# Kernel optimization log

Hardware: AMD Instinct MI355X
Metric: run time of the kernel (lower is better)

The kernel has to match this reference:

```python
import jax, jax.numpy as jnp
import numpy as np

C, I, O = 32, 1024, 1024
B, T = 64, 512


def setup_inputs() -> dict:
    key = jax.random.key(0)
    kx, kc, kw, kb = jax.random.split(key, 4)
    x = jax.random.normal(kx, (B, T, I), dtype=jnp.float32)
    cat_ids = jax.random.randint(kc, (B,), 0, C)
    W = 0.02 * jax.random.normal(kw, (C, I, O), dtype=jnp.float32)
    b = jnp.zeros((C, O), dtype=jnp.float32)
    return {"x": x, "cat_ids": cat_ids, "W": W, "b": b}


def reference(x, cat_ids, W, b):
    # Per-category affine: y[b] = x[b] @ W[cat_ids[b]] + b[cat_ids[b]]
    selected_W = W[cat_ids]            # [B, I, O] (gathered per batch element)
    selected_b = b[cat_ids]            # [B, O]
    if x.ndim == 2:
        return jnp.einsum('bi,bio->bo', x, selected_W) + selected_b
    return jnp.einsum('bti,bio->bto', x, selected_W) + selected_b[:, None, :]
```

## Files before the change

kernel.cpp:

```cpp
#include <hip/hip_runtime.h>
#include <hip/hip_bf16.h>
#include <stdint.h>

#define CATS  32
#define DI    1024
#define DO    1024
#define NB    64
#define ST    512

typedef float  f32x4  __attribute__((ext_vector_type(4)));
typedef short  bf16x8 __attribute__((ext_vector_type(8)));

__device__ __forceinline__ unsigned short f2bf(float f) {
    union { float f; unsigned int u; } v;
    v.f = f;
    unsigned int r = v.u + 0x7FFFu + ((v.u >> 16) & 1u);
    return (unsigned short)(r >> 16);
}

__global__ __launch_bounds__(256) void wt_transpose_kernel(
        const float* __restrict__ W, unsigned short* __restrict__ Wt) {
    __shared__ float tile[128 * 65];
    const int c  = blockIdx.z;
    const int i0 = blockIdx.y * 128;
    const int o0 = blockIdx.x * 64;
    const float* Wc = W + (size_t)c * DI * DO;
    const int tid = threadIdx.x;

    const int f  = tid & 15;
    const int r0 = tid >> 4;
    #pragma unroll
    for (int rr = 0; rr < 8; ++rr) {
        const int r = r0 + rr * 16;
        const f32x4 v = *(const f32x4*)(Wc + (size_t)(i0 + r) * DO + (o0 + 4 * f));
        #pragma unroll
        for (int j = 0; j < 4; ++j)
            tile[r * 65 + 4 * f + j] = v[j];
    }
    __syncthreads();

    const int g   = tid & 15;
    const int ol0 = tid >> 4;
    unsigned short* WtC = Wt + (size_t)c * DO * DI;
    #pragma unroll
    for (int oo = 0; oo < 4; ++oo) {
        const int ol = ol0 + oo * 16;
        unsigned int w[4];
        #pragma unroll
        for (int j = 0; j < 4; ++j) {
            const unsigned short lo = f2bf(tile[(8 * g + 2 * j + 0) * 65 + ol]);
            const unsigned short hi = f2bf(tile[(8 * g + 2 * j + 1) * 65 + ol]);
            w[j] = (unsigned int)lo | ((unsigned int)hi << 16);
        }
        uint4 pk; pk.x = w[0]; pk.y = w[1]; pk.z = w[2]; pk.w = w[3];
        *(uint4*)(WtC + (size_t)(o0 + ol) * DI + (i0 + 8 * g)) = pk;
    }
}

__global__ __launch_bounds__(256) void x_convert_kernel(
        const float* __restrict__ x, unsigned short* __restrict__ xb) {
    const size_t i = ((size_t)blockIdx.x * 256 + threadIdx.x) * 8;
    const f32x4 v0 = *(const f32x4*)(x + i);
    const f32x4 v1 = *(const f32x4*)(x + i + 4);
    uint4 pk;
    pk.x = (unsigned int)f2bf(v0[0]) | ((unsigned int)f2bf(v0[1]) << 16);
    pk.y = (unsigned int)f2bf(v0[2]) | ((unsigned int)f2bf(v0[3]) << 16);
    pk.z = (unsigned int)f2bf(v1[0]) | ((unsigned int)f2bf(v1[1]) << 16);
    pk.w = (unsigned int)f2bf(v1[2]) | ((unsigned int)f2bf(v1[3]) << 16);
    *(uint4*)(xb + i) = pk;
}

#define BM 128
#define BN 128
#define BK 32

__global__ __launch_bounds__(256) void cat_gemm_kernel(
        const unsigned short* __restrict__ xb, const int* __restrict__ cat_ids,
        const unsigned short* __restrict__ Wt, const float* __restrict__ bias,
        float* __restrict__ out) {
    __shared__ __align__(16) unsigned short As[2][BM * BK];
    __shared__ __align__(16) unsigned short Bs[2][BN * BK];

    const int b     = blockIdx.z;
    const int mbase = blockIdx.y * BM;
    const int nbase = blockIdx.x * BN;
    const int cat   = cat_ids[b];

    const int tid  = threadIdx.x;
    const int lane = tid & 63;
    const int w    = tid >> 6;
    const int wr   = w >> 1;
    const int wc   = w & 1;
    const int l15  = lane & 15;
    const int kg   = lane >> 4;

    const int sr     = lane >> 2;
    const int schunk = (lane & 3) ^ ((lane >> 3) & 3);

    const unsigned short* gA = xb + (size_t)(b * ST + mbase) * DI;
    const unsigned short* gB = Wt + ((size_t)cat * DO + nbase) * DI;

    const int koff = (kg ^ ((l15 >> 1) & 3)) * 8;

    f32x4 acc[4][4];
    #pragma unroll
    for (int mi = 0; mi < 4; ++mi)
        #pragma unroll
        for (int ni = 0; ni < 4; ++ni)
            acc[mi][ni] = (f32x4){0.f, 0.f, 0.f, 0.f};

    #define STAGE(bufi, k0)                                                          \
        do {                                                                         \
            _Pragma("unroll")                                                        \
            for (int q = 0; q < 2; ++q) {                                            \
                const int row = w * 32 + q * 16 + sr;                                \
                __builtin_amdgcn_global_load_lds(                                    \
                    (const __attribute__((address_space(1))) void*)                  \
                        (gA + (size_t)row * DI + (k0) + schunk * 8),                 \
                    (__attribute__((address_space(3))) void*)                        \
                        &As[bufi][(w * 32 + q * 16) * BK],                           \
                    16, 0, 0);                                                       \
                __builtin_amdgcn_global_load_lds(                                    \
                    (const __attribute__((address_space(1))) void*)                  \
                        (gB + (size_t)row * DI + (k0) + schunk * 8),                 \
                    (__attribute__((address_space(3))) void*)                        \
                        &Bs[bufi][(w * 32 + q * 16) * BK],                           \
                    16, 0, 0);                                                       \
            }                                                                        \
        } while (0)

    STAGE(0, 0);
    __syncthreads();

    int buf = 0;
    #pragma unroll 1
    for (int step = 0; step < DI / BK; ++step) {
        if (step + 1 < DI / BK)
            STAGE(buf ^ 1, (step + 1) * BK);

        bf16x8 af[4], bf[4];
        #pragma unroll
        for (int mi = 0; mi < 4; ++mi) {
            const int m = wr * 64 + mi * 16 + l15;
            af[mi] = *(const bf16x8*)&As[buf][m * BK + koff];
        }
        #pragma unroll
        for (int ni = 0; ni < 4; ++ni) {
            const int n = wc * 64 + ni * 16 + l15;
            bf[ni] = *(const bf16x8*)&Bs[buf][n * BK + koff];
        }

        #pragma unroll
        for (int mi = 0; mi < 4; ++mi)
            #pragma unroll
            for (int ni = 0; ni < 4; ++ni)
                acc[mi][ni] = __builtin_amdgcn_mfma_f32_16x16x32_bf16(
                                  af[mi], bf[ni], acc[mi][ni], 0, 0, 0);

        __syncthreads();
        buf ^= 1;
    }
    #undef STAGE

    float bs[4];
    #pragma unroll
    for (int ni = 0; ni < 4; ++ni)
        bs[ni] = bias[(size_t)cat * DO + nbase + wc * 64 + ni * 16 + l15];

    #pragma unroll
    for (int mi = 0; mi < 4; ++mi) {
        const int rowb = mbase + wr * 64 + mi * 16 + kg * 4;
        #pragma unroll
        for (int r = 0; r < 4; ++r) {
            float* orow = out + (size_t)(b * ST + rowb + r) * DO
                              + nbase + wc * 64 + l15;
            #pragma unroll
            for (int ni = 0; ni < 4; ++ni)
                orow[ni * 16] = acc[mi][ni][r] + bs[ni];
        }
    }
}

__global__ __launch_bounds__(256) void naive_kernel(
        const float* __restrict__ x, const int* __restrict__ cat_ids,
        const float* __restrict__ W, const float* __restrict__ bias,
        float* __restrict__ out) {
    const int bt = blockIdx.x;
    const int b  = bt >> 9;
    const int t  = bt & 511;
    const int cat = cat_ids[b];
    const float* xr = x + ((size_t)b * ST + t) * DI;
    const float* Wc = W + (size_t)cat * DI * DO;
    const int o = threadIdx.x;
    float a0 = bias[cat * DO + o];
    float a1 = bias[cat * DO + o + 256];
    float a2 = bias[cat * DO + o + 512];
    float a3 = bias[cat * DO + o + 768];
    for (int i = 0; i < DI; ++i) {
        const float xv = xr[i];
        const float* wrow = Wc + (size_t)i * DO;
        a0 += xv * wrow[o];
        a1 += xv * wrow[o + 256];
        a2 += xv * wrow[o + 512];
        a3 += xv * wrow[o + 768];
    }
    float* orow = out + ((size_t)b * ST + t) * DO;
    orow[o] = a0; orow[o + 256] = a1; orow[o + 512] = a2; orow[o + 768] = a3;
}

extern "C" void kernel_launch(void* const* d_in, const int* in_sizes, int n_in,
                              void* d_out, int out_size, void* d_ws, size_t ws_size,
                              hipStream_t stream) {
    const float* x    = (const float*)d_in[0];
    const int*   cats = (const int*)d_in[1];
    const float* W    = (const float*)d_in[2];
    const float* bias = (const float*)d_in[3];
    float*       out  = (float*)d_out;

    const size_t wt_bytes = (size_t)CATS * DI * DO * sizeof(unsigned short);
    const size_t xb_bytes = (size_t)NB * ST * DI * sizeof(unsigned short);

    if (ws_size >= wt_bytes + xb_bytes) {
        unsigned short* Wt = (unsigned short*)d_ws;
        unsigned short* xb = (unsigned short*)((char*)d_ws + wt_bytes);
        wt_transpose_kernel<<<dim3(DO / 64, DI / 128, CATS), 256, 0, stream>>>(W, Wt);
        x_convert_kernel<<<(NB * ST * DI) / (256 * 8), 256, 0, stream>>>(x, xb);
        cat_gemm_kernel<<<dim3(DO / BN, ST / BM, NB), 256, 0, stream>>>(
            xb, cats, Wt, bias, out);
    } else {
        naive_kernel<<<NB * ST, 256, 0, stream>>>(x, cats, W, bias, out);
    }
}
```

Before: 430.9 us.

## Fuse bf16 conversion and weight transpose into the category GEMM main loop

Removes the separate weight transpose and x conversion kernels and their workspace round-trips. The GEMM now loads fp32 x and W through registers, converts them with packed bf16 conversion instructions and writes them into swizzled LDS tiles. This replaces the direct global-to-LDS async loads with register staging. The block index is also remapped so neighbouring blocks share tiles. The trade-off is reading fp32 operands repeatedly from global memory (twice the bytes per tile) and doing conversion work in the inner loop, instead of the one-time preprocessing passes that were removed.

```diff
diff --git a/kernel.cpp b/kernel.cpp
--- a/kernel.cpp
+++ b/kernel.cpp
@@ -1,5 +1,4 @@
 #include <hip/hip_runtime.h>
-#include <hip/hip_bf16.h>
 #include <stdint.h>
 
 #define CATS  32
@@ -8,82 +7,32 @@
 #define NB    64
 #define ST    512
 
+#define BM 128
+#define BN 128
+#define BK 32
+#define NSTEP (DI / BK)
+
 typedef float  f32x4  __attribute__((ext_vector_type(4)));
 typedef short  bf16x8 __attribute__((ext_vector_type(8)));
 
-__device__ __forceinline__ unsigned short f2bf(float f) {
-    union { float f; unsigned int u; } v;
-    v.f = f;
-    unsigned int r = v.u + 0x7FFFu + ((v.u >> 16) & 1u);
-    return (unsigned short)(r >> 16);
+__device__ __forceinline__ uint32_t cvt_pk_bf16(float lo, float hi) {
+    uint32_t r;
+    asm("v_cvt_pk_bf16_f32 %0, %1, %2" : "=v"(r) : "v"(lo), "v"(hi));
+    return r;
 }
 
-__global__ __launch_bounds__(256) void wt_transpose_kernel(
-        const float* __restrict__ W, unsigned short* __restrict__ Wt) {
-    __shared__ float tile[128 * 65];
-    const int c  = blockIdx.z;
-    const int i0 = blockIdx.y * 128;
-    const int o0 = blockIdx.x * 64;
-    const float* Wc = W + (size_t)c * DI * DO;
-    const int tid = threadIdx.x;
-
-    const int f  = tid & 15;
-    const int r0 = tid >> 4;
-    #pragma unroll
-    for (int rr = 0; rr < 8; ++rr) {
-        const int r = r0 + rr * 16;
-        const f32x4 v = *(const f32x4*)(Wc + (size_t)(i0 + r) * DO + (o0 + 4 * f));
-        #pragma unroll
-        for (int j = 0; j < 4; ++j)
-            tile[r * 65 + 4 * f + j] = v[j];
-    }
-    __syncthreads();
-
-    const int g   = tid & 15;
-    const int ol0 = tid >> 4;
-    unsigned short* WtC = Wt + (size_t)c * DO * DI;
-    #pragma unroll
-    for (int oo = 0; oo < 4; ++oo) {
-        const int ol = ol0 + oo * 16;
-        unsigned int w[4];
-        #pragma unroll
-        for (int j = 0; j < 4; ++j) {
-            const unsigned short lo = f2bf(tile[(8 * g + 2 * j + 0) * 65 + ol]);
-            const unsigned short hi = f2bf(tile[(8 * g + 2 * j + 1) * 65 + ol]);
-            w[j] = (unsigned int)lo | ((unsigned int)hi << 16);
-        }
-        uint4 pk; pk.x = w[0]; pk.y = w[1]; pk.z = w[2]; pk.w = w[3];
-        *(uint4*)(WtC + (size_t)(o0 + ol) * DI + (i0 + 8 * g)) = pk;
-    }
-}
-
-__global__ __launch_bounds__(256) void x_convert_kernel(
-        const float* __restrict__ x, unsigned short* __restrict__ xb) {
-    const size_t i = ((size_t)blockIdx.x * 256 + threadIdx.x) * 8;
-    const f32x4 v0 = *(const f32x4*)(x + i);
-    const f32x4 v1 = *(const f32x4*)(x + i + 4);
-    uint4 pk;
-    pk.x = (unsigned int)f2bf(v0[0]) | ((unsigned int)f2bf(v0[1]) << 16);
-    pk.y = (unsigned int)f2bf(v0[2]) | ((unsigned int)f2bf(v0[3]) << 16);
-    pk.z = (unsigned int)f2bf(v1[0]) | ((unsigned int)f2bf(v1[1]) << 16);
-    pk.w = (unsigned int)f2bf(v1[2]) | ((unsigned int)f2bf(v1[3]) << 16);
-    *(uint4*)(xb + i) = pk;
-}
-
-#define BM 128
-#define BN 128
-#define BK 32
-
-__global__ __launch_bounds__(256) void cat_gemm_kernel(
-        const unsigned short* __restrict__ xb, const int* __restrict__ cat_ids,
-        const unsigned short* __restrict__ Wt, const float* __restrict__ bias,
+__global__ __launch_bounds__(256) void fused_cat_gemm_kernel(
+        const float* __restrict__ x, const int* __restrict__ cat_ids,
+        const float* __restrict__ W, const float* __restrict__ bias,
         float* __restrict__ out) {
     __shared__ __align__(16) unsigned short As[2][BM * BK];
     __shared__ __align__(16) unsigned short Bs[2][BN * BK];
 
-    const int b     = blockIdx.z;
-    const int mbase = blockIdx.y * BM;
-    const int nbase = blockIdx.x * BN;
+    const int fb = blockIdx.x;
+    const int vv = (fb & 7) * 256 + (fb >> 3);
+    const int b     = vv >> 5;
+    const int mbase = ((vv >> 3) & 3) * BM;
+    const int nbase = (vv & 7) * BN;
     const int cat   = cat_ids[b];
 
     const int tid  = threadIdx.x;
@@ -93,14 +42,17 @@
     const int wc   = w & 1;
     const int l15  = lane & 15;
     const int kg   = lane >> 4;
+    const int koff = (kg ^ ((l15 >> 1) & 3)) * 8;
 
-    const int sr     = lane >> 2;
-    const int schunk = (lane & 3) ^ ((lane >> 3) & 3);
+    const int am   = tid >> 3;
+    const int ak   = (tid & 7) * 4;
+    const int ac   = (ak >> 3) ^ ((am >> 1) & 3);
+    const int aoff = am * BK + ac * 8 + (ak & 4);
+    const float* gA = x + (size_t)(b * ST + mbase + am) * DI + ak;
 
-    const unsigned short* gA = xb + (size_t)(b * ST + mbase) * DI;
-    const unsigned short* gB = Wt + ((size_t)cat * DO + nbase) * DI;
-
-    const int koff = (kg ^ ((l15 >> 1) & 3)) * 8;
+    const int nq  = tid & 31;
+    const int k2b = tid >> 5;
+    const float* gB = W + (size_t)cat * DI * DO + nbase + nq * 4;
 
     f32x4 acc[4][4];
     #pragma unroll
@@ -109,63 +61,78 @@
         for (int ni = 0; ni < 4; ++ni)
             acc[mi][ni] = (f32x4){0.f, 0.f, 0.f, 0.f};
 
-    #define STAGE(bufi, k0)                                                          \
-        do {                                                                         \
-            _Pragma("unroll")                                                        \
-            for (int q = 0; q < 2; ++q) {                                            \
-                const int row = w * 32 + q * 16 + sr;                                \
-                __builtin_amdgcn_global_load_lds(                                    \
-                    (const __attribute__((address_space(1))) void*)                  \
-                        (gA + (size_t)row * DI + (k0) + schunk * 8),                 \
-                    (__attribute__((address_space(3))) void*)                        \
-                        &As[bufi][(w * 32 + q * 16) * BK],                           \
-                    16, 0, 0);                                                       \
-                __builtin_amdgcn_global_load_lds(                                    \
-                    (const __attribute__((address_space(1))) void*)                  \
-                        (gB + (size_t)row * DI + (k0) + schunk * 8),                 \
-                    (__attribute__((address_space(3))) void*)                        \
-                        &Bs[bufi][(w * 32 + q * 16) * BK],                           \
-                    16, 0, 0);                                                       \
-            }                                                                        \
-        } while (0)
+    f32x4 ra[4];
+    f32x4 rb0[2], rb1[2];
 
-    STAGE(0, 0);
+    auto LOADS = [&](int step) {
+        #pragma unroll
+        for (int q = 0; q < 4; ++q)
+            ra[q] = *(const f32x4*)(gA + (size_t)q * 32 * DI + step * BK);
+        #pragma unroll
+        for (int u = 0; u < 2; ++u) {
+            const float* p = gB + (size_t)(step * BK + (k2b + 8 * u) * 2) * DO;
+            rb0[u] = *(const f32x4*)p;
+            rb1[u] = *(const f32x4*)(p + DO);
+        }
+    };
+
+    auto WRITES = [&](int bufi) {
+        #pragma unroll
+        for (int q = 0; q < 4; ++q) {
+            uint2 pk;
+            pk.x = cvt_pk_bf16(ra[q][0], ra[q][1]);
+            pk.y = cvt_pk_bf16(ra[q][2], ra[q][3]);
+            *(uint2*)&As[bufi][aoff + q * 32 * BK] = pk;
+        }
+        #pragma unroll
+        for (int u = 0; u < 2; ++u) {
+            const int k2 = k2b + 8 * u;
+            #pragma unroll
+            for (int j = 0; j < 4; ++j) {
+                const int n = nq * 4 + j;
+                const int c = (k2 >> 2) ^ ((n >> 1) & 3);
+                *(uint32_t*)&Bs[bufi][n * BK + c * 8 + (k2 & 3) * 2] =
+                    cvt_pk_bf16(rb0[u][j], rb1[u][j]);
+            }
+        }
+    };
+
+    LOADS(0);
+    WRITES(0);
     __syncthreads();
 
     int buf = 0;
     #pragma unroll 1
-    for (int step = 0; step < DI / BK; ++step) {
-        if (step + 1 < DI / BK)
-            STAGE(buf ^ 1, (step + 1) * BK);
+    for (int step = 0; step < NSTEP; ++step) {
+        if (step + 1 < NSTEP)
+            LOADS(step + 1);
 
-        bf16x8 af[4], bf[4];
+        bf16x8 af[4], bfr[4];
         #pragma unroll
-        for (int mi = 0; mi < 4; ++mi) {
-            const int m = wr * 64 + mi * 16 + l15;
-            af[mi] = *(const bf16x8*)&As[buf][m * BK + koff];
-        }
+        for (int mi = 0; mi < 4; ++mi)
+            af[mi] = *(const bf16x8*)&As[buf][(wr * 64 + mi * 16 + l15) * BK + koff];
         #pragma unroll
-        for (int ni = 0; ni < 4; ++ni) {
-            const int n = wc * 64 + ni * 16 + l15;
-            bf[ni] = *(const bf16x8*)&Bs[buf][n * BK + koff];
-        }
+        for (int ni = 0; ni < 4; ++ni)
+            bfr[ni] = *(const bf16x8*)&Bs[buf][(wc * 64 + ni * 16 + l15) * BK + koff];
 
         #pragma unroll
         for (int mi = 0; mi < 4; ++mi)
             #pragma unroll
             for (int ni = 0; ni < 4; ++ni)
                 acc[mi][ni] = __builtin_amdgcn_mfma_f32_16x16x32_bf16(
-                                  af[mi], bf[ni], acc[mi][ni], 0, 0, 0);
+                                  af[mi], bfr[ni], acc[mi][ni], 0, 0, 0);
+
+        if (step + 1 < NSTEP)
+            WRITES(buf ^ 1);
 
         __syncthreads();
         buf ^= 1;
     }
-    #undef STAGE
 
-    float bs[4];
+    float bsv[4];
     #pragma unroll
     for (int ni = 0; ni < 4; ++ni)
-        bs[ni] = bias[(size_t)cat * DO + nbase + wc * 64 + ni * 16 + l15];
+        bsv[ni] = bias[(size_t)cat * DO + nbase + wc * 64 + ni * 16 + l15];
 
     #pragma unroll
     for (int mi = 0; mi < 4; ++mi) {
@@ -176,36 +143,9 @@
                               + nbase + wc * 64 + l15;
             #pragma unroll
             for (int ni = 0; ni < 4; ++ni)
-                orow[ni * 16] = acc[mi][ni][r] + bs[ni];
+                orow[ni * 16] = acc[mi][ni][r] + bsv[ni];
         }
     }
-}
-
-__global__ __launch_bounds__(256) void naive_kernel(
-        const float* __restrict__ x, const int* __restrict__ cat_ids,
-        const float* __restrict__ W, const float* __restrict__ bias,
-        float* __restrict__ out) {
-    const int bt = blockIdx.x;
-    const int b  = bt >> 9;
-    const int t  = bt & 511;
-    const int cat = cat_ids[b];
-    const float* xr = x + ((size_t)b * ST + t) * DI;
-    const float* Wc = W + (size_t)cat * DI * DO;
-    const int o = threadIdx.x;
-    float a0 = bias[cat * DO + o];
-    float a1 = bias[cat * DO + o + 256];
-    float a2 = bias[cat * DO + o + 512];
-    float a3 = bias[cat * DO + o + 768];
-    for (int i = 0; i < DI; ++i) {
-        const float xv = xr[i];
-        const float* wrow = Wc + (size_t)i * DO;
-        a0 += xv * wrow[o];
-        a1 += xv * wrow[o + 256];
-        a2 += xv * wrow[o + 512];
-        a3 += xv * wrow[o + 768];
-    }
-    float* orow = out + ((size_t)b * ST + t) * DO;
-    orow[o] = a0; orow[o + 256] = a1; orow[o + 512] = a2; orow[o + 768] = a3;
 }
 
 extern "C" void kernel_launch(void* const* d_in, const int* in_sizes, int n_in,
@@ -217,17 +157,8 @@
     const float* bias = (const float*)d_in[3];
     float*       out  = (float*)d_out;
 
-    const size_t wt_bytes = (size_t)CATS * DI * DO * sizeof(unsigned short);
-    const size_t xb_bytes = (size_t)NB * ST * DI * sizeof(unsigned short);
+    (void)d_ws; (void)ws_size;
 
-    if (ws_size >= wt_bytes + xb_bytes) {
-        unsigned short* Wt = (unsigned short*)d_ws;
-        unsigned short* xb = (unsigned short*)((char*)d_ws + wt_bytes);
-        wt_transpose_kernel<<<dim3(DO / 64, DI / 128, CATS), 256, 0, stream>>>(W, Wt);
-        x_convert_kernel<<<(NB * ST * DI) / (256 * 8), 256, 0, stream>>>(x, xb);
-        cat_gemm_kernel<<<dim3(DO / BN, ST / BM, NB), 256, 0, stream>>>(
-            xb, cats, Wt, bias, out);
-    } else {
-        naive_kernel<<<NB * ST, 256, 0, stream>>>(x, cats, W, bias, out);
-    }
+    fused_cat_gemm_kernel<<<NB * (ST / BM) * (DO / BN), 256, 0, stream>>>(
+        x, cats, W, bias, out);
 }
```

Result: no change. 428.9 us (-0.5%).
